# Performance work log

Hardware: AMD Instinct MI355X
Metric: run time of the kernel (lower is better)

Reference implementation:

```python
import jax, jax.numpy as jnp
import numpy as np

H = 8            # heads
HD = 32          # head dim (projection_dim // heads)
E = 256          # embedding dim
L = 343          # window length (7^3)
NW = 128         # number of windows
B = 1            # batch
CPB_HID = 512


def setup_inputs() -> dict:
    key = jax.random.key(0)
    ks = jax.random.split(key, 16)
    s = 0.02
    inp = {
        "query": jax.random.normal(ks[0], (B, NW, L, E), jnp.float32),
        "key": jax.random.normal(ks[1], (B, NW, L, E), jnp.float32),
        "value": jax.random.normal(ks[2], (B, NW, L, E), jnp.float32),
        # integer 3D relative offsets in [-6, 6], cast to float for the CPB MLP
        "indices": jax.random.randint(ks[3], (L, L, 3), -6, 7).astype(jnp.float32),
        "mask": jax.random.bernoulli(ks[4], 0.1, (1, NW, 1, L, L)),
        "Wq": jax.random.normal(ks[5], (E, H * HD), jnp.float32) * s,
        "bq": jnp.zeros((H * HD,), jnp.float32),
        "Wk": jax.random.normal(ks[6], (E, H * HD), jnp.float32) * s,
        "bk": jnp.zeros((H * HD,), jnp.float32),
        "Wv": jax.random.normal(ks[7], (E, H * HD), jnp.float32) * s,
        "Ww": jax.random.normal(ks[8], (H * HD, E), jnp.float32) * s,
        "bw_proj": jnp.zeros((E,), jnp.float32),
        "scale": jnp.ones((1,), jnp.float32),
        "W1": jax.random.normal(ks[9], (3, CPB_HID), jnp.float32) * s,
        "b1": jnp.zeros((CPB_HID,), jnp.float32),
        "W2": jax.random.normal(ks[10], (CPB_HID, H), jnp.float32) * s,
        "b2": jnp.zeros((H,), jnp.float32),
    }
    return inp


def _l2norm(x):
    # matches torch F.normalize(dim=-1, eps=1e-12)
    n = jnp.linalg.norm(x, axis=-1, keepdims=True)
    return x / jnp.maximum(n, 1e-12)


def reference(query, key, value, indices, mask, Wq, bq, Wk, bk, Wv, Ww, bw_proj,
              scale, W1, b1, W2, b2):
    b, nw, l, e = query.shape
    bb = b * nw
    q = query.reshape(bb, l, e)
    k = key.reshape(bb, l, e)
    v = value.reshape(bb, l, e)
    # projections -> (bb, H, L, HD)
    def split_heads(x):
        return x.reshape(bb, l, H, HD).transpose(0, 2, 1, 3)
    pq = split_heads(q @ Wq + bq)
    pk = split_heads(k @ Wk + bk)
    pv = split_heads(v @ Wv)  # no bias on V
    # cosine-similarity attention with learned temperature
    nq = _l2norm(pq)
    nk = _l2norm(pk)
    ctx = jnp.einsum('bhnc,bhmc->bhnm', nq, nk) / jnp.maximum(scale, 0.01)[0]
    # log-spaced continuous position bias via small MLP
    log_idx = jnp.sign(indices) * jnp.log2(1.0 + jnp.abs(indices)) / jnp.log2(jnp.float32(8.0))
    hid = jax.nn.relu(log_idx @ W1 + b1)               # (L, L, 512)
    bias = 16.0 * jax.nn.sigmoid(hid @ W2 + b2)        # (L, L, H)
    ctx = ctx + bias.transpose(2, 0, 1)[None]          # (bb, H, L, L)
    # shifted-window mask
    ctx = ctx.reshape(b, nw, H, l, l)
    ctx = jnp.where(mask, jnp.float32(-100000.0), ctx)
    ctx = ctx.reshape(bb, H, l, l)
    attn = jax.nn.softmax(ctx, axis=-1)
    out = jnp.einsum('bhnm,bhmc->bhnc', attn, pv)
    out = out.transpose(0, 2, 1, 3).reshape(bb, l, H * HD)
    out = out @ Ww + bw_proj
    return out.reshape(b, nw, l, e)
```

## Files before the change

### kernel.cpp

```cpp
#include <hip/hip_runtime.h>
#include <hip/hip_bf16.h>

typedef unsigned short u16;
typedef unsigned int u32;
typedef unsigned long long u64;
typedef float f32x4 __attribute__((ext_vector_type(4)));
typedef u16 u16x8 __attribute__((ext_vector_type(8)));
typedef _Float16 h16x8 __attribute__((ext_vector_type(8)));

#define L_ 343
#define LL_ 117649
#define H_ 8
#define HD_ 32
#define NW_ 128
#define LP_ 352
#define NF_ 22
#define NKST 40
#define VTST 360
#define PMW 12

__device__ __forceinline__ u16 f2h(float f) {
    _Float16 h = (_Float16)f;
    return __builtin_bit_cast(u16, h);
}

__global__ __launch_bounds__(256) void cvtw_kernel(
    const float* __restrict__ Wq, const float* __restrict__ Wk,
    const float* __restrict__ Wv, const float* __restrict__ Ww,
    u16* __restrict__ wt)
{
    const float* Ws[4] = {Wq, Wk, Wv, Ww};
    const int mat = blockIdx.y;
    const float* W = Ws[mat];
    int idx = blockIdx.x * 256 + threadIdx.x;
    int n  = idx >> 6;
    int kb = (idx & 63) * 4;
    u16* d = wt + mat * 65536 + n * 256 + kb;
    #pragma unroll
    for (int j = 0; j < 4; ++j)
        d[j] = f2h(W[(kb + j) * 256 + n]);
}

__global__ __launch_bounds__(256) void cpb_table_kernel(
    const float* __restrict__ W1, const float* __restrict__ b1,
    const float* __restrict__ W2, const float* __restrict__ b2,
    float* __restrict__ table)
{
    __shared__ float red[256 * 9];
    const int e = blockIdx.x;
    const int t = threadIdx.x;
    int t0 = e / 169, rem = e % 169, t1 = rem / 13, t2 = rem % 13;
    int tt[3] = {t0, t1, t2};
    float li[3];
    #pragma unroll
    for (int i = 0; i < 3; ++i) {
        float c = (float)(tt[i] - 6);
        li[i] = copysignf(log2f(1.0f + fabsf(c)) * (1.0f / 3.0f), c);
    }
    float p[8] = {0,0,0,0,0,0,0,0};
    for (int jj = t; jj < 512; jj += 256) {
        float hs = li[0]*W1[jj] + li[1]*W1[512+jj] + li[2]*W1[1024+jj] + b1[jj];
        float hid = fmaxf(hs, 0.0f);
        #pragma unroll
        for (int o = 0; o < 8; ++o) p[o] += hid * W2[jj*8 + o];
    }
    #pragma unroll
    for (int o = 0; o < 8; ++o) red[t*9 + o] = p[o];
    __syncthreads();
    for (int s = 128; s > 0; s >>= 1) {
        if (t < s) {
            #pragma unroll
            for (int o = 0; o < 8; ++o) red[t*9+o] += red[(t+s)*9+o];
        }
        __syncthreads();
    }
    if (t < 8)
        table[e*8 + t] = 16.0f / (1.0f + __expf(-(red[t] + b2[t])));
}

__global__ __launch_bounds__(256) void e16_kernel(
    const float* __restrict__ idxf, u16* __restrict__ e16)
{
    int g = blockIdx.x * 256 + threadIdx.x;
    if (g >= LL_) return;
    int a = (int)idxf[g*3 + 0] + 6;
    int b = (int)idxf[g*3 + 1] + 6;
    int c = (int)idxf[g*3 + 2] + 6;
    e16[g] = (u16)((a * 13 + b) * 13 + c);
}

__global__ __launch_bounds__(256) void pack_mask_kernel(
    const u32* __restrict__ m32, u64* __restrict__ pm)
{
    bool isU8 = false;
    for (int i = 0; i < 64; ++i)
        if (m32[i] & 0xFFFFFF00u) isU8 = true;
    const unsigned char* m8 = (const unsigned char*)m32;
    int row = blockIdx.x * 4 + (threadIdx.x >> 6);
    int lane = threadIdx.x & 63;
    #pragma unroll
    for (int pass = 0; pass < 6; ++pass) {
        int j = pass * 64 + lane;
        int val = 0;
        if (j < L_)
            val = isU8 ? (int)m8[(size_t)row * L_ + j] : (int)m32[(size_t)row * L_ + j];
        u64 bits = __ballot(val != 0);
        if (lane == 0) pm[(size_t)row * 6 + pass] = bits;
    }
}

__global__ __launch_bounds__(256) void proj_kernel(
    const float* __restrict__ qx, const float* __restrict__ kx, const float* __restrict__ vx,
    const u16* __restrict__ wt, const float* __restrict__ bq, const float* __restrict__ bk,
    const float* __restrict__ scale,
    u16* __restrict__ pq, u16* __restrict__ pk, u16* __restrict__ pv)
{
    __shared__ u16 Al[64 * NKST];
    __shared__ u16 Bl[256 * NKST];
    const int mt = blockIdx.x, which = blockIdx.y, w = blockIdx.z;
    const float* X   = (which == 0) ? qx : ((which == 1) ? kx : vx);
    const u16* WT    = wt + which * 65536;
    const float* bias= (which == 0) ? bq : ((which == 1) ? bk : nullptr);
    u16* dst         = (which == 0) ? pq : ((which == 1) ? pk : pv);
    const int tid = threadIdx.x;
    const int wid = tid >> 6, lane = tid & 63, lr = lane & 15, lg = lane >> 4;
    const int r0 = tid >> 2, q4 = (tid & 3) * 8;
    const float* Xb = X + (size_t)w * L_ * 256;
    const f32x4 fz = {0.f, 0.f, 0.f, 0.f};
    f32x4 acc[4][4];
    #pragma unroll
    for (int i = 0; i < 4; ++i)
        #pragma unroll
        for (int j = 0; j < 4; ++j) acc[i][j] = fz;

    for (int kk = 0; kk < 8; ++kk) {
        __syncthreads();
        {
            int row = mt * 64 + r0;
            u16x8 u = {0,0,0,0,0,0,0,0};
            if (row < L_) {
                const float* s = Xb + row * 256 + kk * 32 + q4;
                f32x4 a = *(const f32x4*)s;
                f32x4 b = *(const f32x4*)(s + 4);
                #pragma unroll
                for (int j = 0; j < 4; ++j) { u[j] = f2h(a[j]); u[4+j] = f2h(b[j]); }
            }
            *(u16x8*)(&Al[r0 * NKST + q4]) = u;
        }
        {
            const u16* s = WT + tid * 256 + kk * 32;
            u16x8 b0 = *(const u16x8*)(s);
            u16x8 b1 = *(const u16x8*)(s + 8);
            u16x8 b2 = *(const u16x8*)(s + 16);
            u16x8 b3 = *(const u16x8*)(s + 24);
            u16* d = &Bl[tid * NKST];
            *(u16x8*)(d)      = b0;
            *(u16x8*)(d + 8)  = b1;
            *(u16x8*)(d + 16) = b2;
            *(u16x8*)(d + 24) = b3;
        }
        __syncthreads();
        h16x8 af[4];
        #pragma unroll
        for (int rf = 0; rf < 4; ++rf)
            af[rf] = *(const h16x8*)(&Al[(rf*16 + lr) * NKST + lg*8]);
        #pragma unroll
        for (int nf = 0; nf < 4; ++nf) {
            h16x8 b8 = *(const h16x8*)(&Bl[(wid*64 + nf*16 + lr) * NKST + lg*8]);
            #pragma unroll
            for (int rf = 0; rf < 4; ++rf)
                acc[rf][nf] = __builtin_amdgcn_mfma_f32_16x16x32_f16(af[rf], b8, acc[rf][nf], 0, 0, 0);
        }
    }
    const float sv = 1.0f / fmaxf(scale[0], 0.01f);
    #pragma unroll
    for (int hh = 0; hh < 2; ++hh) {
        const int h = 2 * wid + hh;
        float b0v = 0.f, b1v = 0.f;
        if (bias) { b0v = bias[h * 32 + lr]; b1v = bias[h * 32 + 16 + lr]; }
        #pragma unroll
        for (int rf = 0; rf < 4; ++rf) {
            #pragma unroll
            for (int reg = 0; reg < 4; ++reg) {
                float a0 = acc[rf][2*hh][reg] + b0v;
                float a1 = acc[rf][2*hh+1][reg] + b1v;
                float inv = 1.0f;
                if (which < 2) {
                    float ss = a0*a0 + a1*a1;
                    ss += __shfl_xor(ss, 1); ss += __shfl_xor(ss, 2);
                    ss += __shfl_xor(ss, 4); ss += __shfl_xor(ss, 8);
                    inv = 1.0f / fmaxf(sqrtf(ss), 1e-12f);
                    if (which == 0) inv *= sv;
                }
                int row = mt * 64 + rf * 16 + lg * 4 + reg;
                if (row < L_) {
                    u16* d = dst + (((size_t)w * H_ + h) * L_ + row) * HD_;
                    d[lr]      = f2h(a0 * inv);
                    d[16 + lr] = f2h(a1 * inv);
                }
            }
        }
    }
}

__global__ __launch_bounds__(256) void attn_kernel(
    const u16* __restrict__ pq, const u16* __restrict__ pk, const u16* __restrict__ pv,
    const float* __restrict__ table, const u16* __restrict__ e16,
    const u32* __restrict__ pm32, u16* __restrict__ ao)
{
    __shared__ u16 nk[LP_ * NKST];
    __shared__ u16 vT[HD_ * VTST];
    __shared__ u16 nq[64 * NKST];
    __shared__ u16 Pw[4][16 * NKST];
    __shared__ float tableh[2197];

    const int h = blockIdx.x, w = blockIdx.y;
    const int tid = threadIdx.x;
    const int wid = tid >> 6, lane = tid & 63;
    const int lr = lane & 15, lg = lane >> 4;
    const u16* pkb = pk + ((size_t)(w * H_ + h)) * L_ * HD_;
    const u16* pvb = pv + ((size_t)(w * H_ + h)) * L_ * HD_;
    const u16* pqb = pq + ((size_t)(w * H_ + h)) * L_ * HD_;
    const int r0 = tid >> 2, q4 = (tid & 3) * 8;
    const f32x4 fz = {0.f, 0.f, 0.f, 0.f};

    for (int i = tid; i < 2197; i += 256) tableh[i] = table[i * 8 + h];

    #pragma unroll
    for (int pass = 0; pass < 6; ++pass) {
        int r = pass * 64 + r0;
        if (r < LP_) {
            u16x8 u = {0,0,0,0,0,0,0,0};
            if (r < L_) u = *(const u16x8*)(pkb + r * HD_ + q4);
            *(u16x8*)(&nk[r * NKST + q4]) = u;
        }
    }
    #pragma unroll
    for (int pass = 0; pass < 6; ++pass) {
        int r = pass * 64 + r0;
        if (r < LP_) {
            u16x8 u = {0,0,0,0,0,0,0,0};
            if (r < L_) u = *(const u16x8*)(pvb + r * HD_ + q4);
            #pragma unroll
            for (int j = 0; j < 8; ++j) vT[(q4 + j) * VTST + r] = u[j];
        }
    }

    for (int qt = 0; qt < 6; ++qt) {
        const int qbase = qt * 64;
        __syncthreads();
        {
            int r = qbase + r0;
            u16x8 u = {0,0,0,0,0,0,0,0};
            if (r < L_) u = *(const u16x8*)(pqb + r * HD_ + q4);
            *(u16x8*)(&nq[r0 * NKST + q4]) = u;
        }
        __syncthreads();

        h16x8 aq = *(const h16x8*)(&nq[(wid * 16 + lr) * NKST + lg * 8]);
        f32x4 S[NF_];
        #pragma unroll
        for (int f = 0; f < NF_; ++f) {
            h16x8 b8 = *(const h16x8*)(&nk[(f * 16 + lr) * NKST + lg * 8]);
            S[f] = __builtin_amdgcn_mfma_f32_16x16x32_f16(aq, b8, fz, 0, 0, 0);
        }

        const int rbase = qbase + wid * 16 + lg * 4;
        float mx[4] = {-1e30f, -1e30f, -1e30f, -1e30f};
        #pragma unroll
        for (int reg = 0; reg < 4; ++reg) {
            int row = rbase + reg;
            int br = (row < L_) ? row : (L_ - 1);
            const u16* er = e16 + (size_t)br * L_;
            const u32* pmrow = pm32 + ((size_t)w * L_ + br) * PMW;
            #pragma unroll
            for (int f = 0; f < NF_; ++f) {
                int col = f * 16 + lr;
                float lo;
                if (col < L_) {
                    lo = S[f][reg] + tableh[er[col]];
                    if ((pmrow[f >> 1] >> ((f & 1) * 16 + lr)) & 1) lo = -100000.0f;
                } else {
                    lo = -1e30f;
                }
                S[f][reg] = lo;
                mx[reg] = fmaxf(mx[reg], lo);
            }
        }
        #pragma unroll
        for (int reg = 0; reg < 4; ++reg)
            for (int d = 1; d < 16; d <<= 1)
                mx[reg] = fmaxf(mx[reg], __shfl_xor(mx[reg], d));
        float sm[4] = {0.f, 0.f, 0.f, 0.f};
        #pragma unroll
        for (int f = 0; f < NF_; ++f)
            #pragma unroll
            for (int reg = 0; reg < 4; ++reg) {
                float e = __expf(S[f][reg] - mx[reg]);
                S[f][reg] = e;
                sm[reg] += e;
            }
        #pragma unroll
        for (int reg = 0; reg < 4; ++reg)
            for (int d = 1; d < 16; d <<= 1)
                sm[reg] += __shfl_xor(sm[reg], d);
        float rv[4];
        #pragma unroll
        for (int reg = 0; reg < 4; ++reg) rv[reg] = 1.0f / sm[reg];

        f32x4 O0 = fz, O1 = fz;
        u16* Pm = &Pw[wid][0];
        #pragma unroll
        for (int cc = 0; cc < 11; ++cc) {
            #pragma unroll
            for (int half = 0; half < 2; ++half) {
                int f = cc * 2 + half;
                #pragma unroll
                for (int reg = 0; reg < 4; ++reg)
                    Pm[(lg * 4 + reg) * NKST + half * 16 + lr] = f2h(S[f][reg] * rv[reg]);
            }
            h16x8 pa = *(const h16x8*)(&Pm[lr * NKST + lg * 8]);
            h16x8 v0 = *(const h16x8*)(&vT[lr * VTST + cc * 32 + lg * 8]);
            h16x8 v1 = *(const h16x8*)(&vT[(16 + lr) * VTST + cc * 32 + lg * 8]);
            O0 = __builtin_amdgcn_mfma_f32_16x16x32_f16(pa, v0, O0, 0, 0, 0);
            O1 = __builtin_amdgcn_mfma_f32_16x16x32_f16(pa, v1, O1, 0, 0, 0);
        }
        #pragma unroll
        for (int reg = 0; reg < 4; ++reg) {
            int row = rbase + reg;
            if (row < L_) {
                size_t o = ((size_t)w * L_ + row) * 256 + h * HD_;
                ao[o + lr]      = f2h(O0[reg]);
                ao[o + 16 + lr] = f2h(O1[reg]);
            }
        }
    }
}

__global__ __launch_bounds__(256) void outproj_kernel(
    const u16* __restrict__ ao, const u16* __restrict__ WT,
    const float* __restrict__ bw, float* __restrict__ out)
{
    __shared__ u16 Al[64 * NKST];
    __shared__ u16 Bl[256 * NKST];
    const int mt = blockIdx.x;
    const int tid = threadIdx.x;
    const int wid = tid >> 6, lane = tid & 63, lr = lane & 15, lg = lane >> 4;
    const int r0 = tid >> 2, q4 = (tid & 3) * 8;
    const f32x4 fz = {0.f, 0.f, 0.f, 0.f};
    f32x4 acc[4][4];
    #pragma unroll
    for (int i = 0; i < 4; ++i)
        #pragma unroll
        for (int j = 0; j < 4; ++j) acc[i][j] = fz;

    for (int kk = 0; kk < 8; ++kk) {
        __syncthreads();
        {
            int row = mt * 64 + r0;
            u16x8 u = *(const u16x8*)(ao + (size_t)row * 256 + kk * 32 + q4);
            *(u16x8*)(&Al[r0 * NKST + q4]) = u;
        }
        {
            const u16* s = WT + tid * 256 + kk * 32;
            u16x8 b0 = *(const u16x8*)(s);
            u16x8 b1 = *(const u16x8*)(s + 8);
            u16x8 b2 = *(const u16x8*)(s + 16);
            u16x8 b3 = *(const u16x8*)(s + 24);
            u16* d = &Bl[tid * NKST];
            *(u16x8*)(d)      = b0;
            *(u16x8*)(d + 8)  = b1;
            *(u16x8*)(d + 16) = b2;
            *(u16x8*)(d + 24) = b3;
        }
        __syncthreads();
        h16x8 af[4];
        #pragma unroll
        for (int rf = 0; rf < 4; ++rf)
            af[rf] = *(const h16x8*)(&Al[(rf*16 + lr) * NKST + lg*8]);
        #pragma unroll
        for (int nf = 0; nf < 4; ++nf) {
            h16x8 b8 = *(const h16x8*)(&Bl[(wid*64 + nf*16 + lr) * NKST + lg*8]);
            #pragma unroll
            for (int rf = 0; rf < 4; ++rf)
                acc[rf][nf] = __builtin_amdgcn_mfma_f32_16x16x32_f16(af[rf], b8, acc[rf][nf], 0, 0, 0);
        }
    }
    #pragma unroll
    for (int nf = 0; nf < 4; ++nf) {
        int col = wid * 64 + nf * 16 + lr;
        float bv = bw[col];
        #pragma unroll
        for (int rf = 0; rf < 4; ++rf) {
            #pragma unroll
            for (int reg = 0; reg < 4; ++reg) {
                int row = mt * 64 + rf * 16 + lg * 4 + reg;
                out[(size_t)row * 256 + col] = acc[rf][nf][reg] + bv;
            }
        }
    }
}

extern "C" void kernel_launch(void* const* d_in, const int* in_sizes, int n_in,
                              void* d_out, int out_size, void* d_ws, size_t ws_size,
                              hipStream_t stream) {
    const float* q    = (const float*)d_in[0];
    const float* k    = (const float*)d_in[1];
    const float* v    = (const float*)d_in[2];
    const float* idxf = (const float*)d_in[3];
    const u32*   mask = (const u32*)d_in[4];
    const float* Wq   = (const float*)d_in[5];
    const float* bq   = (const float*)d_in[6];
    const float* Wk   = (const float*)d_in[7];
    const float* bk   = (const float*)d_in[8];
    const float* Wv   = (const float*)d_in[9];
    const float* Ww   = (const float*)d_in[10];
    const float* bw   = (const float*)d_in[11];
    const float* scale= (const float*)d_in[12];
    const float* W1   = (const float*)d_in[13];
    const float* b1   = (const float*)d_in[14];
    const float* W2   = (const float*)d_in[15];
    const float* b2   = (const float*)d_in[16];
    float* out = (float*)d_out;

    char* ws = (char*)d_ws;
    size_t off = 0;
    auto take = [&](size_t nbytes) -> void* {
        void* p = (void*)(ws + off);
        off += (nbytes + 255) & ~(size_t)255;
        return p;
    };
    u16*   wt    = (u16*)  take((size_t)4 * 65536 * 2);
    float* table = (float*)take((size_t)2197 * 8 * 4);
    u16*   e16   = (u16*)  take((size_t)LL_ * 2);
    u64*   pm    = (u64*)  take((size_t)NW_ * L_ * 6 * 8);
    const size_t PN = (size_t)NW_ * H_ * L_ * HD_;
    u16* pq = (u16*)take(PN * 2);
    u16* pk = (u16*)take(PN * 2);
    u16* pv = (u16*)take(PN * 2);
    u16* ao = (u16*)take(PN * 2);
    if (off > ws_size) return;

    hipLaunchKernelGGL(cvtw_kernel, dim3(64, 4), dim3(256), 0, stream, Wq, Wk, Wv, Ww, wt);
    hipLaunchKernelGGL(cpb_table_kernel, dim3(2197), dim3(256), 0, stream, W1, b1, W2, b2, table);
    hipLaunchKernelGGL(e16_kernel, dim3((LL_ + 255) / 256), dim3(256), 0, stream, idxf, e16);
    hipLaunchKernelGGL(pack_mask_kernel, dim3(NW_ * L_ / 4), dim3(256), 0, stream, mask, pm);
    hipLaunchKernelGGL(proj_kernel, dim3(6, 3, NW_), dim3(256), 0, stream,
                       q, k, v, wt, bq, bk, scale, pq, pk, pv);
    hipLaunchKernelGGL(attn_kernel, dim3(H_, NW_), dim3(256), 0, stream,
                       pq, pk, pv, table, e16, (const u32*)pm, ao);
    hipLaunchKernelGGL(outproj_kernel, dim3(686), dim3(256), 0, stream,
                       ao, wt + 3 * 65536, bw, out);
}
```

Baseline: 523.8 us.

## Precompute per-head bias matrix, split attention query tiles across two blocks, swizzle LDS

Adds a kernel that expands the CPB table into a dense per-head padded bias matrix, so attention reads the bias directly instead of doing an index lookup into a shared-memory table. The attention grid gains a z dimension of 2, with each block handling 3 of the 6 query tiles, which doubles parallelism. Q is now loaded straight from global memory rather than staged in LDS. The K, V^T and P shared-memory layouts are re-laid out with padding offsets to reduce bank conflicts, and launch bounds request higher occupancy. The CPB table reduction now uses wave shuffles. The costs are a larger bias buffer read from global or L2 and K/V being loaded twice per head-window.

```diff
diff --git a/kernel.cpp b/kernel.cpp
--- a/kernel.cpp
+++ b/kernel.cpp
@@ -16,8 +16,10 @@
 #define LP_ 352
 #define NF_ 22
 #define NKST 40
-#define VTST 360
 #define PMW 12
+#define BCP 352
+#define NKC 2832
+#define VTS 360
 
 __device__ __forceinline__ u16 f2h(float f) {
     _Float16 h = (_Float16)f;
@@ -46,9 +48,10 @@
     const float* __restrict__ W2, const float* __restrict__ b2,
     float* __restrict__ table)
 {
-    __shared__ float red[256 * 9];
+    __shared__ float red[4 * 8];
     const int e = blockIdx.x;
     const int t = threadIdx.x;
+    const int wid = t >> 6, lane = t & 63;
     int t0 = e / 169, rem = e % 169, t1 = rem / 13, t2 = rem % 13;
     int tt[3] = {t0, t1, t2};
     float li[3];
@@ -65,17 +68,18 @@
         for (int o = 0; o < 8; ++o) p[o] += hid * W2[jj*8 + o];
     }
     #pragma unroll
-    for (int o = 0; o < 8; ++o) red[t*9 + o] = p[o];
+    for (int o = 0; o < 8; ++o) {
+        for (int d = 1; d < 64; d <<= 1) p[o] += __shfl_xor(p[o], d);
+    }
+    if (lane == 0) {
+        #pragma unroll
+        for (int o = 0; o < 8; ++o) red[wid * 8 + o] = p[o];
+    }
     __syncthreads();
-    for (int s = 128; s > 0; s >>= 1) {
-        if (t < s) {
-            #pragma unroll
-            for (int o = 0; o < 8; ++o) red[t*9+o] += red[(t+s)*9+o];
-        }
-        __syncthreads();
-    }
-    if (t < 8)
-        table[e*8 + t] = 16.0f / (1.0f + __expf(-(red[t] + b2[t])));
+    if (t < 8) {
+        float s = red[t] + red[8 + t] + red[16 + t] + red[24 + t] + b2[t];
+        table[e*8 + t] = 16.0f / (1.0f + __expf(-s));
+    }
 }
 
 __global__ __launch_bounds__(256) void e16_kernel(
@@ -87,6 +91,19 @@
     int b = (int)idxf[g*3 + 1] + 6;
     int c = (int)idxf[g*3 + 2] + 6;
     e16[g] = (u16)((a * 13 + b) * 13 + c);
+}
+
+__global__ __launch_bounds__(256) void biasx_kernel(
+    const u16* __restrict__ e16, const float* __restrict__ table,
+    float* __restrict__ biasv)
+{
+    const int i = blockIdx.x;
+    const int hh = blockIdx.y;
+    for (int j = threadIdx.x; j < BCP; j += 256) {
+        float v = 0.f;
+        if (j < L_) v = table[(int)e16[i * L_ + j] * 8 + hh];
+        biasv[((size_t)hh * L_ + i) * BCP + j] = v;
+    }
 }
 
 __global__ __launch_bounds__(256) void pack_mask_kernel(
@@ -203,86 +220,74 @@
     }
 }
 
-__global__ __launch_bounds__(256) void attn_kernel(
+__global__ __launch_bounds__(256, 3) void attn_kernel(
     const u16* __restrict__ pq, const u16* __restrict__ pk, const u16* __restrict__ pv,
-    const float* __restrict__ table, const u16* __restrict__ e16,
-    const u32* __restrict__ pm32, u16* __restrict__ ao)
-{
-    __shared__ u16 nk[LP_ * NKST];
-    __shared__ u16 vT[HD_ * VTST];
-    __shared__ u16 nq[64 * NKST];
-    __shared__ u16 Pw[4][16 * NKST];
-    __shared__ float tableh[2197];
-
-    const int h = blockIdx.x, w = blockIdx.y;
+    const float* __restrict__ biasv, const u32* __restrict__ pm32,
+    u16* __restrict__ ao)
+{
+    __shared__ u16 nk[4 * NKC];
+    __shared__ u16 vT[32 * VTS + 48];
+    __shared__ u16 Pw[4][784];
+
+    const int h = blockIdx.x, w = blockIdx.y, z = blockIdx.z;
     const int tid = threadIdx.x;
     const int wid = tid >> 6, lane = tid & 63;
     const int lr = lane & 15, lg = lane >> 4;
     const u16* pkb = pk + ((size_t)(w * H_ + h)) * L_ * HD_;
     const u16* pvb = pv + ((size_t)(w * H_ + h)) * L_ * HD_;
     const u16* pqb = pq + ((size_t)(w * H_ + h)) * L_ * HD_;
+    const float* biash = biasv + (size_t)h * L_ * BCP;
     const int r0 = tid >> 2, q4 = (tid & 3) * 8;
     const f32x4 fz = {0.f, 0.f, 0.f, 0.f};
 
-    for (int i = tid; i < 2197; i += 256) tableh[i] = table[i * 8 + h];
-
+    const int kcb = (q4 >> 3) * NKC;
+    const int vtb = q4 * VTS + (q4 >> 3) * 16;
     #pragma unroll
     for (int pass = 0; pass < 6; ++pass) {
         int r = pass * 64 + r0;
         if (r < LP_) {
             u16x8 u = {0,0,0,0,0,0,0,0};
             if (r < L_) u = *(const u16x8*)(pkb + r * HD_ + q4);
-            *(u16x8*)(&nk[r * NKST + q4]) = u;
-        }
-    }
-    #pragma unroll
-    for (int pass = 0; pass < 6; ++pass) {
-        int r = pass * 64 + r0;
-        if (r < LP_) {
-            u16x8 u = {0,0,0,0,0,0,0,0};
-            if (r < L_) u = *(const u16x8*)(pvb + r * HD_ + q4);
-            #pragma unroll
-            for (int j = 0; j < 8; ++j) vT[(q4 + j) * VTST + r] = u[j];
-        }
-    }
-
-    for (int qt = 0; qt < 6; ++qt) {
-        const int qbase = qt * 64;
-        __syncthreads();
-        {
-            int r = qbase + r0;
-            u16x8 u = {0,0,0,0,0,0,0,0};
-            if (r < L_) u = *(const u16x8*)(pqb + r * HD_ + q4);
-            *(u16x8*)(&nq[r0 * NKST + q4]) = u;
-        }
-        __syncthreads();
-
-        h16x8 aq = *(const h16x8*)(&nq[(wid * 16 + lr) * NKST + lg * 8]);
+            *(u16x8*)(&nk[kcb + r * 8]) = u;
+            u16x8 v = {0,0,0,0,0,0,0,0};
+            if (r < L_) v = *(const u16x8*)(pvb + r * HD_ + q4);
+            #pragma unroll
+            for (int j = 0; j < 8; ++j) vT[vtb + j * VTS + r] = v[j];
+        }
+    }
+    __syncthreads();
+
+    u16* Pm = &Pw[wid][0];
+    const int pwb = lr * 40 + (lr >> 2) * 48 + lg * 8;
+    const int v0b = lr * VTS + (lr >> 3) * 16;
+    const int v1b = (16 + lr) * VTS + (2 + (lr >> 3)) * 16;
+
+    for (int qt = 0; qt < 3; ++qt) {
+        const int qbase = z * 192 + qt * 64;
+        const int rbase = qbase + wid * 16 + lg * 4;
+
+        h16x8 aq = *(const h16x8*)(pqb + (qbase + wid * 16 + lr) * HD_ + lg * 8);
+
         f32x4 S[NF_];
         #pragma unroll
         for (int f = 0; f < NF_; ++f) {
-            h16x8 b8 = *(const h16x8*)(&nk[(f * 16 + lr) * NKST + lg * 8]);
+            h16x8 b8 = *(const h16x8*)(&nk[lg * NKC + (f * 16 + lr) * 8]);
             S[f] = __builtin_amdgcn_mfma_f32_16x16x32_f16(aq, b8, fz, 0, 0, 0);
         }
 
-        const int rbase = qbase + wid * 16 + lg * 4;
         float mx[4] = {-1e30f, -1e30f, -1e30f, -1e30f};
         #pragma unroll
         for (int reg = 0; reg < 4; ++reg) {
             int row = rbase + reg;
             int br = (row < L_) ? row : (L_ - 1);
-            const u16* er = e16 + (size_t)br * L_;
+            const float* brow = biash + (size_t)br * BCP;
             const u32* pmrow = pm32 + ((size_t)w * L_ + br) * PMW;
             #pragma unroll
             for (int f = 0; f < NF_; ++f) {
                 int col = f * 16 + lr;
-                float lo;
-                if (col < L_) {
-                    lo = S[f][reg] + tableh[er[col]];
-                    if ((pmrow[f >> 1] >> ((f & 1) * 16 + lr)) & 1) lo = -100000.0f;
-                } else {
-                    lo = -1e30f;
-                }
+                float lo = S[f][reg] + brow[col];
+                if ((pmrow[f >> 1] >> ((f & 1) * 16 + lr)) & 1) lo = -100000.0f;
+                if (f == NF_ - 1 && col >= L_) lo = -1e30f;
                 S[f][reg] = lo;
                 mx[reg] = fmaxf(mx[reg], lo);
             }
@@ -309,7 +314,6 @@
         for (int reg = 0; reg < 4; ++reg) rv[reg] = 1.0f / sm[reg];
 
         f32x4 O0 = fz, O1 = fz;
-        u16* Pm = &Pw[wid][0];
         #pragma unroll
         for (int cc = 0; cc < 11; ++cc) {
             #pragma unroll
@@ -317,11 +321,11 @@
                 int f = cc * 2 + half;
                 #pragma unroll
                 for (int reg = 0; reg < 4; ++reg)
-                    Pm[(lg * 4 + reg) * NKST + half * 16 + lr] = f2h(S[f][reg] * rv[reg]);
-            }
-            h16x8 pa = *(const h16x8*)(&Pm[lr * NKST + lg * 8]);
-            h16x8 v0 = *(const h16x8*)(&vT[lr * VTST + cc * 32 + lg * 8]);
-            h16x8 v1 = *(const h16x8*)(&vT[(16 + lr) * VTST + cc * 32 + lg * 8]);
+                    Pm[(lg * 4 + reg) * 40 + lg * 48 + half * 16 + lr] = f2h(S[f][reg] * rv[reg]);
+            }
+            h16x8 pa = *(const h16x8*)(&Pm[pwb]);
+            h16x8 v0 = *(const h16x8*)(&vT[v0b + cc * 32 + lg * 8]);
+            h16x8 v1 = *(const h16x8*)(&vT[v1b + cc * 32 + lg * 8]);
             O0 = __builtin_amdgcn_mfma_f32_16x16x32_f16(pa, v0, O0, 0, 0, 0);
             O1 = __builtin_amdgcn_mfma_f32_16x16x32_f16(pa, v1, O1, 0, 0, 0);
         }
@@ -433,6 +437,7 @@
     u16*   wt    = (u16*)  take((size_t)4 * 65536 * 2);
     float* table = (float*)take((size_t)2197 * 8 * 4);
     u16*   e16   = (u16*)  take((size_t)LL_ * 2);
+    float* biasv = (float*)take((size_t)H_ * L_ * BCP * 4);
     u64*   pm    = (u64*)  take((size_t)NW_ * L_ * 6 * 8);
     const size_t PN = (size_t)NW_ * H_ * L_ * HD_;
     u16* pq = (u16*)take(PN * 2);
@@ -444,11 +449,12 @@
     hipLaunchKernelGGL(cvtw_kernel, dim3(64, 4), dim3(256), 0, stream, Wq, Wk, Wv, Ww, wt);
     hipLaunchKernelGGL(cpb_table_kernel, dim3(2197), dim3(256), 0, stream, W1, b1, W2, b2, table);
     hipLaunchKernelGGL(e16_kernel, dim3((LL_ + 255) / 256), dim3(256), 0, stream, idxf, e16);
+    hipLaunchKernelGGL(biasx_kernel, dim3(L_, H_), dim3(256), 0, stream, e16, table, biasv);
     hipLaunchKernelGGL(pack_mask_kernel, dim3(NW_ * L_ / 4), dim3(256), 0, stream, mask, pm);
     hipLaunchKernelGGL(proj_kernel, dim3(6, 3, NW_), dim3(256), 0, stream,
                        q, k, v, wt, bq, bk, scale, pq, pk, pv);
-    hipLaunchKernelGGL(attn_kernel, dim3(H_, NW_), dim3(256), 0, stream,
-                       pq, pk, pv, table, e16, (const u32*)pm, ao);
+    hipLaunchKernelGGL(attn_kernel, dim3(H_, NW_, 2), dim3(256), 0, stream,
+                       pq, pk, pv, biasv, (const u32*)pm, ao);
     hipLaunchKernelGGL(outproj_kernel, dim3(686), dim3(256), 0, stream,
                        ao, wt + 3 * 65536, bw, out);
 }
```

Result: slower. 569.7 us (+8.8%).
